# Kernel tuning notes

Measured on AMD Instinct MI355X. Metric: run time of the kernel, lower is better.

The kernel has to match this reference:

```python
import jax, jax.numpy as jnp
import numpy as np

N = 50000      # n_nodes
E = 800000     # edges (before self-loops)
IN = 128       # in_dim
HID = 32       # hidden_dim (per-head out channels)
HEADS = 4
EMB = 128      # embed_dim
LAYERS = 3
NEG_SLOPE = 0.2  # PyG GATv2 default leaky_relu slope


def _layer_norm(x, g, b):
    mu = jnp.mean(x, axis=-1, keepdims=True)
    var = jnp.var(x, axis=-1, keepdims=True)
    return g * (x - mu) / jnp.sqrt(var + 1e-5) + b


def _gatv2(h, src, dst, n, Wl, bl, Wr, br, att, bias):
    # GATv2Conv (PyG semantics, share_weights=False, concat=True).
    H, C = att.shape
    xl = (h @ Wl + bl).reshape(n, H, C)   # target (i) transform
    xr = (h @ Wr + br).reshape(n, H, C)   # source (j) transform
    x_i = xl[dst]                          # [Etot, H, C] gather
    x_j = xr[src]
    e = jax.nn.leaky_relu(x_i + x_j, NEG_SLOPE)
    logit = jnp.einsum('ehc,hc->eh', e, att)          # [Etot, H]
    # segment softmax over destination node (every node has a self-loop)
    m = jax.ops.segment_max(logit, dst, num_segments=n)
    ex = jnp.exp(logit - m[dst])
    den = jax.ops.segment_sum(ex, dst, num_segments=n)
    alpha = ex / (den[dst] + 1e-16)
    out = jax.ops.segment_sum(alpha[..., None] * x_j, dst, num_segments=n)
    return out.reshape(n, H * C) + bias


def setup_inputs() -> dict:
    key = jax.random.key(0)
    ks = iter(jax.random.split(key, 64))
    d = {}
    d['x'] = jax.random.normal(next(ks), (N, IN), jnp.float32)
    d['edge_index'] = jax.random.randint(next(ks), (2, E), 0, N, dtype=jnp.int64)

    def w(shape, fan):
        return jax.random.normal(next(ks), shape, jnp.float32) / np.float32(np.sqrt(fan))

    HC = HID * HEADS
    d['W_in'] = w((IN, HID), IN); d['b_in'] = jnp.zeros((HID,), jnp.float32)
    for i in range(LAYERS):
        ic = HID if i == 0 else HC
        d[f'Wl{i}'] = w((ic, HC), ic); d[f'bl{i}'] = jnp.zeros((HC,), jnp.float32)
        d[f'Wr{i}'] = w((ic, HC), ic); d[f'br{i}'] = jnp.zeros((HC,), jnp.float32)
        d[f'att{i}'] = w((HEADS, HID), HID)
        d[f'bo{i}'] = jnp.zeros((HC,), jnp.float32)
        d[f'g{i}'] = jnp.ones((HC,), jnp.float32)
        d[f'be{i}'] = jnp.zeros((HC,), jnp.float32)
    d['W_out'] = w((HC, EMB), HC); d['b_out'] = jnp.zeros((EMB,), jnp.float32)
    return d


def reference(x, edge_index, W_in, b_in,
              Wl0, bl0, Wr0, br0, att0, bo0, g0, be0,
              Wl1, bl1, Wr1, br1, att1, bo1, g1, be1,
              Wl2, bl2, Wr2, br2, att2, bo2, g2, be2,
              W_out, b_out):
    n = x.shape[0]
    loops = jnp.arange(n, dtype=edge_index.dtype)  # add_self_loops=True
    src = jnp.concatenate([edge_index[0], loops])
    dst = jnp.concatenate([edge_index[1], loops])

    h = jax.nn.gelu(x @ W_in + b_in, approximate=False)
    layers = [(Wl0, bl0, Wr0, br0, att0, bo0, g0, be0),
              (Wl1, bl1, Wr1, br1, att1, bo1, g1, be1),
              (Wl2, bl2, Wr2, br2, att2, bo2, g2, be2)]
    for (Wl, bl, Wr, br, att, bo, g, be) in layers:
        h_new = jax.nn.gelu(_layer_norm(_gatv2(h, src, dst, n, Wl, bl, Wr, br, att, bo), g, be), approximate=False)
        h = h + h_new if h.shape == h_new.shape else h_new  # dropout = identity (eval)
    out = h @ W_out + b_out
    norm = jnp.maximum(jnp.linalg.norm(out, axis=-1, keepdims=True), 1e-12)
    return out / norm
```

## Files before the change

### kernel.cpp

```cpp
#include <hip/hip_runtime.h>
#include <hip/hip_bf16.h>
#include <math.h>

#define N_NODES 50000
#define N_EDGES 800000
#define IN_DIM  128
#define HC_DIM  128
#define HID_C   32
#define SCAN_NB 196
#define LOG2E   1.4426950408889634f

typedef __attribute__((ext_vector_type(8))) short short8;
typedef __attribute__((ext_vector_type(4))) float f32x4;
typedef _Float16 hf8 __attribute__((ext_vector_type(8)));
typedef unsigned int uint4v __attribute__((ext_vector_type(4)));

__device__ __forceinline__ float gelu_f(float x){
    return 0.5f*x*(1.0f + erff(x*0.7071067811865475f));
}

__device__ __forceinline__ void split2(float f, short& h, short& l){
    __hip_bfloat16 bh = __float2bfloat16(f);
    float r = f - __bfloat162float(bh);
    __hip_bfloat16 blo = __float2bfloat16(r);
    h = *reinterpret_cast<short*>(&bh);
    l = *reinterpret_cast<short*>(&blo);
}
__device__ __forceinline__ unsigned short f2h(float f){
    _Float16 h = (_Float16)f;
    return __builtin_bit_cast(unsigned short, h);
}
__device__ __forceinline__ float bf2f(unsigned short u){
    return __uint_as_float(((unsigned)u)<<16);
}

__global__ __launch_bounds__(256) void k_count(const int* __restrict__ dst, int* __restrict__ cnt,
                                               int* __restrict__ rank){
    int b = blockIdx.x*1024 + threadIdx.x;
    #pragma unroll
    for(int i=0;i<4;i++){
        int e = b + i*256;
        if(e < N_EDGES) rank[e] = atomicAdd(&cnt[dst[e]], 1);
    }
}

__global__ __launch_bounds__(256) void k_scan1(const int* __restrict__ cnt, int* __restrict__ rowptr,
                                               int* __restrict__ part){
    __shared__ int sh[256];
    int t=threadIdx.x; int i=blockIdx.x*256+t;
    int v = (i<N_NODES)? cnt[i] : 0;
    sh[t]=v; __syncthreads();
    for(int off=1; off<256; off<<=1){
        int y = (t>=off)? sh[t-off] : 0;
        __syncthreads();
        sh[t] += y;
        __syncthreads();
    }
    if(i<N_NODES) rowptr[i] = sh[t]-v;
    if(t==255) part[blockIdx.x] = sh[255];
}

__global__ __launch_bounds__(256) void k_scan2(int* __restrict__ part){
    __shared__ int sh[256];
    int t=threadIdx.x;
    int v = (t<SCAN_NB)? part[t] : 0;
    sh[t]=v; __syncthreads();
    for(int off=1; off<256; off<<=1){
        int y=(t>=off)? sh[t-off]:0;
        __syncthreads();
        sh[t]+=y;
        __syncthreads();
    }
    if(t<SCAN_NB) part[t] = sh[t]-v;
}

__global__ __launch_bounds__(256) void k_scan3(int* __restrict__ rowptr, const int* __restrict__ part){
    int t=threadIdx.x; int i=blockIdx.x*256+t;
    if(i<N_NODES) rowptr[i] += part[blockIdx.x];
    if(i==0) rowptr[N_NODES]=N_EDGES;
}

__global__ __launch_bounds__(256) void k_fill(const int* __restrict__ src, const int* __restrict__ dst,
                                              const int* __restrict__ rowptr, const int* __restrict__ rank,
                                              int* __restrict__ col){
    int b = blockIdx.x*1024 + threadIdx.x;
    #pragma unroll
    for(int i=0;i<4;i++){
        int e = b + i*256;
        if(e < N_EDGES) col[rowptr[dst[e]] + rank[e]] = src[e];
    }
}

__global__ __launch_bounds__(256) void k_splitW(const float* __restrict__ W0, const float* __restrict__ W1,
                                                const float* __restrict__ W2, const float* __restrict__ W3,
                                                const float* __restrict__ W4, const float* __restrict__ W5,
                                                const float* __restrict__ W6, short* __restrict__ WT){
    int bx = blockIdx.x;
    int m, kc;
    if(bx < 2){ m = bx; kc = 0; }
    else { m = 2 + (bx-2)/4; kc = (bx-2)&3; }
    const float* src; int K; size_t off;
    switch(m){
        case 0: src=W0; K=32;  off=0;      break;
        case 1: src=W1; K=32;  off=8192;   break;
        case 2: src=W2; K=128; off=16384;  break;
        case 3: src=W3; K=128; off=49152;  break;
        case 4: src=W4; K=128; off=81920;  break;
        case 5: src=W5; K=128; off=114688; break;
        default:src=W6; K=128; off=147456; break;
    }
    short* hi = WT + off;
    short* lo = hi + (size_t)K*HC_DIM;
    #pragma unroll
    for(int i=0;i<16;i++){
        int idx = threadIdx.x + i*256;
        int k = kc*32 + (idx>>7);
        int n = idx & 127;
        float f = src[(size_t)k*HC_DIM + n];
        short h,l; split2(f,h,l);
        hi[(size_t)n*K + k] = h;
        lo[(size_t)n*K + k] = l;
    }
}

__global__ __launch_bounds__(256) void k_gemm_in(const float* __restrict__ x, const float* __restrict__ W,
                                                 const float* __restrict__ b,
                                                 short* __restrict__ hhi, short* __restrict__ hlo){
    int id = blockIdx.x*256+threadIdx.x;
    int r = id>>5, c = id&31;
    const float4* x4 = (const float4*)(x + (size_t)r*IN_DIM);
    float acc=0.f;
    #pragma unroll 8
    for(int k=0;k<IN_DIM/4;k++){
        float4 xv = x4[k];
        acc = fmaf(xv.x, W[(4*k  )*HID_C+c], acc);
        acc = fmaf(xv.y, W[(4*k+1)*HID_C+c], acc);
        acc = fmaf(xv.z, W[(4*k+2)*HID_C+c], acc);
        acc = fmaf(xv.w, W[(4*k+3)*HID_C+c], acc);
    }
    float v = gelu_f(acc + b[c]);
    short hh,ll; split2(v,hh,ll);
    hhi[(size_t)r*HID_C+c] = hh;
    hlo[(size_t)r*HID_C+c] = ll;
}

template<int K, bool PAIR, bool NORM>
__global__ __launch_bounds__(256) void k_mm(const short* __restrict__ Ahi, const short* __restrict__ Alo,
                                            const short* __restrict__ WTl, const float* __restrict__ bl,
                                            const short* __restrict__ WTr, const float* __restrict__ br,
                                            float* __restrict__ XLf, unsigned short* __restrict__ XLh,
                                            unsigned short* __restrict__ XR16){
    __shared__ float ssq[NORM?256:1];
    int t = threadIdx.x;
    int lane = t & 63, wave = t >> 6;
    int quad = lane >> 4, ml = lane & 15;
    int rbase = blockIdx.x * 64;

    const short* WTl_lo = WTl + (size_t)K*HC_DIM;
    const short* WTr_lo = PAIR ? (WTr + (size_t)K*HC_DIM) : nullptr;

    f32x4 accL[4][2], accR[4][2];
    #pragma unroll
    for(int i=0;i<4;i++)
        #pragma unroll
        for(int j=0;j<2;j++){ accL[i][j]=(f32x4){0,0,0,0}; accR[i][j]=(f32x4){0,0,0,0}; }

    int rowA[4];
    #pragma unroll
    for(int i=0;i<4;i++){
        int rr = rbase + 16*i + ml;
        rowA[i] = (rr < N_NODES) ? rr : (N_NODES-1);
    }

    #pragma unroll 2
    for(int c=0; c<K/32; c++){
        int k0 = c*32 + quad*8;
        short8 ah[4], al[4];
        #pragma unroll
        for(int i=0;i<4;i++){
            ah[i] = *(const short8*)(Ahi + (size_t)rowA[i]*K + k0);
            al[i] = *(const short8*)(Alo + (size_t)rowA[i]*K + k0);
        }
        #pragma unroll
        for(int j=0;j<2;j++){
            int nrow = j*64 + wave*16 + ml;
            short8 bh  = *(const short8*)(WTl    + (size_t)nrow*K + k0);
            short8 blo = *(const short8*)(WTl_lo + (size_t)nrow*K + k0);
            #pragma unroll
            for(int i=0;i<4;i++){
                accL[i][j] = __builtin_amdgcn_mfma_f32_16x16x32_bf16(ah[i], bh,  accL[i][j], 0,0,0);
                accL[i][j] = __builtin_amdgcn_mfma_f32_16x16x32_bf16(ah[i], blo, accL[i][j], 0,0,0);
                accL[i][j] = __builtin_amdgcn_mfma_f32_16x16x32_bf16(al[i], bh,  accL[i][j], 0,0,0);
            }
            if(PAIR){
                short8 ch = *(const short8*)(WTr    + (size_t)nrow*K + k0);
                short8 cl = *(const short8*)(WTr_lo + (size_t)nrow*K + k0);
                #pragma unroll
                for(int i=0;i<4;i++){
                    accR[i][j] = __builtin_amdgcn_mfma_f32_16x16x32_bf16(ah[i], ch, accR[i][j], 0,0,0);
                    accR[i][j] = __builtin_amdgcn_mfma_f32_16x16x32_bf16(ah[i], cl, accR[i][j], 0,0,0);
                    accR[i][j] = __builtin_amdgcn_mfma_f32_16x16x32_bf16(al[i], ch, accR[i][j], 0,0,0);
                }
            }
        }
    }

    int col0 = wave*16 + ml, col1 = 64 + wave*16 + ml;
    float bL0 = bl[col0], bL1 = bl[col1];

    if(NORM){
        #pragma unroll
        for(int i=0;i<4;i++){
            #pragma unroll
            for(int rr=0;rr<4;rr++){
                float v0 = accL[i][0][rr] + bL0;
                float v1 = accL[i][1][rr] + bL1;
                float p = v0*v0 + v1*v1;
                p += __shfl_xor(p,1); p += __shfl_xor(p,2);
                p += __shfl_xor(p,4); p += __shfl_xor(p,8);
                if(ml==0) ssq[wave*64 + 16*i + quad*4 + rr] = p;
            }
        }
        __syncthreads();
        #pragma unroll
        for(int i=0;i<4;i++){
            #pragma unroll
            for(int rr=0;rr<4;rr++){
                int row = 16*i + quad*4 + rr;
                int grr = rbase + row;
                if(grr < N_NODES){
                    float tot = ssq[row] + ssq[64+row] + ssq[128+row] + ssq[192+row];
                    float inv = 1.0f / fmaxf(sqrtf(tot), 1e-12f);
                    XLf[(size_t)grr*HC_DIM + col0] = (accL[i][0][rr] + bL0) * inv;
                    XLf[(size_t)grr*HC_DIM + col1] = (accL[i][1][rr] + bL1) * inv;
                }
            }
        }
    } else {
        float bR0 = PAIR ? br[col0] : 0.f, bR1 = PAIR ? br[col1] : 0.f;
        #pragma unroll
        for(int i=0;i<4;i++){
            #pragma unroll
            for(int rr=0;rr<4;rr++){
                int grr = rbase + 16*i + quad*4 + rr;
                if(grr < N_NODES){
                    XLh[(size_t)grr*HC_DIM + col0] = f2h(accL[i][0][rr] + bL0);
                    XLh[(size_t)grr*HC_DIM + col1] = f2h(accL[i][1][rr] + bL1);
                    if(PAIR){
                        XR16[(size_t)grr*HC_DIM + col0] = f2h(accR[i][0][rr] + bR0);
                        XR16[(size_t)grr*HC_DIM + col1] = f2h(accR[i][1][rr] + bR1);
                    }
                }
            }
        }
    }
}

__global__ __launch_bounds__(256) void k_node(const unsigned short* __restrict__ XLH, const unsigned short* __restrict__ XR,
    const int* __restrict__ rowptr, const int* __restrict__ colidx,
    const float* __restrict__ att, const float* __restrict__ bo,
    const float* __restrict__ gg, const float* __restrict__ be,
    const short* __restrict__ hold_hi, const short* __restrict__ hold_lo,
    short* __restrict__ hi_out, short* __restrict__ lo_out)
{
    int wave=threadIdx.x>>6, lane=threadIdx.x&63;
    int node = blockIdx.x*4+wave;
    int qd = lane >> 4, cl = lane & 15;
    int c8 = cl << 3;
    int ch2 = c8 + (qd<<1);

    #define H2(v,k) __builtin_shufflevector(v, v, 2*(k), 2*(k)+1)
    #define LOADH(j, xv) { xv = *(const hf8*)((const _Float16*)XR + ((size_t)((unsigned)(j)<<7)) + c8); }
#if defined(__has_builtin) && __has_builtin(__builtin_amdgcn_fdot2)
    #define LOGIT(xv, q) { \
        hf8 u_ = xlh + xv; \
        hf8 a_ = __builtin_bit_cast(hf8, __builtin_bit_cast(uint4v, u_) & 0x7fff7fffu); \
        float qa_ = __builtin_amdgcn_fdot2(H2(u_,0), H2(av6,0), 0.f, false); \
        float qb_ = __builtin_amdgcn_fdot2(H2(a_,0), H2(av4,0), 0.f, false); \
        qa_ = __builtin_amdgcn_fdot2(H2(u_,1), H2(av6,1), qa_, false); \
        qb_ = __builtin_amdgcn_fdot2(H2(a_,1), H2(av4,1), qb_, false); \
        qa_ = __builtin_amdgcn_fdot2(H2(u_,2), H2(av6,2), qa_, false); \
        qb_ = __builtin_amdgcn_fdot2(H2(a_,2), H2(av4,2), qb_, false); \
        qa_ = __builtin_amdgcn_fdot2(H2(u_,3), H2(av6,3), qa_, false); \
        qb_ = __builtin_amdgcn_fdot2(H2(a_,3), H2(av4,3), qb_, false); \
        q = qa_ + qb_; \
        q += __shfl_xor(q,1); q += __shfl_xor(q,2); }
#else
    #define LOGIT(xv, q) { \
        hf8 u_ = xlh + xv; \
        hf8 a_ = __builtin_bit_cast(hf8, __builtin_bit_cast(uint4v, u_) & 0x7fff7fffu); \
        q = 0.f; \
        _Pragma("unroll") \
        for(int k_=0;k_<8;k_++) q = fmaf((float)u_[k_], (float)av6[k_], fmaf((float)a_[k_], (float)av4[k_], q)); \
        q += __shfl_xor(q,1); q += __shfl_xor(q,2); }
#endif
    #define UPDATE4 { \
        float nm = fmaxf(m, fmaxf(fmaxf(q0,q1),fmaxf(q2,q3))); \
        float sc = exp2f(m-nm); \
        float e0=exp2f(q0-nm), e1=exp2f(q1-nm), e2=exp2f(q2-nm), e3=exp2f(q3-nm); \
        ls = fmaf(ls, sc, (e0+e1)+(e2+e3)); \
        _Pragma("unroll") \
        for(int k=0;k<8;k++) \
            acc[k] = fmaf(acc[k], sc, fmaf(e0,(float)x0[k], fmaf(e1,(float)x1[k], fmaf(e2,(float)x2[k], e3*(float)x3[k])))); \
        m = nm; }

    int beg = rowptr[node], end = rowptr[node+1];
    hf8 xlh = *(const hf8*)((const _Float16*)XLH + ((size_t)((unsigned)node<<7)) + c8);
    hf8 xs; LOADH(node, xs)
    float hres0 = 0.f, hres1 = 0.f;
    if(hold_hi){
        short2 hh = *(const short2*)(hold_hi + (size_t)node*HC_DIM + ch2);
        short2 hl = *(const short2*)(hold_lo + (size_t)node*HC_DIM + ch2);
        hres0 = bf2f((unsigned short)hh.x) + bf2f((unsigned short)hl.x);
        hres1 = bf2f((unsigned short)hh.y) + bf2f((unsigned short)hl.y);
    }

    float4 aa = *(const float4*)(att + c8);
    float4 abv = *(const float4*)(att + c8 + 4);
    float af[8] = {aa.x,aa.y,aa.z,aa.w,abv.x,abv.y,abv.z,abv.w};
    hf8 av6, av4;
    const float s6 = 0.6f*LOG2E, s4 = 0.4f*LOG2E;
    #pragma unroll
    for(int k=0;k<8;k++){
        av6[k] = (_Float16)(af[k]*s6);
        av4[k] = (_Float16)(af[k]*s4);
    }

    float qs; LOGIT(xs, qs)
    float m, ls, acc[8];
    if(qd==0){
        m = qs; ls = 1.f;
        #pragma unroll
        for(int k=0;k<8;k++) acc[k] = (float)xs[k];
    } else {
        m = -1e30f; ls = 0.f;
        #pragma unroll
        for(int k=0;k<8;k++) acc[k] = 0.f;
    }

    int P = end - beg;
    int nb = P >> 4;
    int base = beg;
    int qoff = qd << 2;
    for(int b=0; b<nb; b++, base += 16){
        int b2 = base + qoff;
        int j0 = colidx[b2], j1 = colidx[b2+1], j2 = colidx[b2+2], j3 = colidx[b2+3];
        hf8 x0,x1,x2,x3;
        LOADH(j0,x0) LOADH(j1,x1) LOADH(j2,x2) LOADH(j3,x3)
        float q0,q1,q2,q3;
        LOGIT(x0,q0) LOGIT(x1,q1) LOGIT(x2,q2) LOGIT(x3,q3)
        UPDATE4
    }
    if(base < end){
        int b2 = base + qoff;
        int j0 = (b2  <end)? colidx[b2]   : node;
        int j1 = (b2+1<end)? colidx[b2+1] : node;
        int j2 = (b2+2<end)? colidx[b2+2] : node;
        int j3 = (b2+3<end)? colidx[b2+3] : node;
        hf8 x0,x1,x2,x3;
        LOADH(j0,x0) LOADH(j1,x1) LOADH(j2,x2) LOADH(j3,x3)
        float q0,q1,q2,q3;
        LOGIT(x0,q0) LOGIT(x1,q1) LOGIT(x2,q2) LOGIT(x3,q3)
        if(b2+1>=end) q1 = -INFINITY;
        if(b2+2>=end) q2 = -INFINITY;
        if(b2+3>=end) q3 = -INFINITY;
        if(b2 < end){
            UPDATE4
        }
    }
    #undef UPDATE4
    #undef LOGIT
    #undef LOADH
    #undef H2

    #pragma unroll
    for(int mk=16; mk<=32; mk<<=1){
        float mo  = __shfl_xor(m, mk);
        float lso = __shfl_xor(ls, mk);
        float ao[8];
        #pragma unroll
        for(int k=0;k<8;k++) ao[k] = __shfl_xor(acc[k], mk);
        float nm = fmaxf(m, mo);
        float s0 = exp2f(m-nm), s1 = exp2f(mo-nm);
        ls = ls*s0 + lso*s1;
        #pragma unroll
        for(int k=0;k<8;k++) acc[k] = acc[k]*s0 + ao[k]*s1;
        m = nm;
    }

    float inv = 1.0f/ls;
    float4 b0 = *(const float4*)(bo + c8);
    float4 b1 = *(const float4*)(bo + c8 + 4);
    float bof[8] = {b0.x,b0.y,b0.z,b0.w,b1.x,b1.y,b1.z,b1.w};
    float o[8];
    #pragma unroll
    for(int k=0;k<8;k++) o[k] = fmaf(acc[k], inv, bof[k]);
    float s1v = ((o[0]+o[1])+(o[2]+o[3])) + ((o[4]+o[5])+(o[6]+o[7]));
    float s2v = o[0]*o[0];
    #pragma unroll
    for(int k=1;k<8;k++) s2v = fmaf(o[k],o[k],s2v);
    #pragma unroll
    for(int mk=1;mk<16;mk<<=1){ s1v += __shfl_xor(s1v,mk); s2v += __shfl_xor(s2v,mk); }
    float mean = s1v*(1.f/128.f);
    float var  = s2v*(1.f/128.f) - mean*mean;
    float rstd = rsqrtf(var + 1e-5f);

    float oa = (qd&2) ? ((qd&1)? o[6] : o[4]) : ((qd&1)? o[2] : o[0]);
    float ob = (qd&2) ? ((qd&1)? o[7] : o[5]) : ((qd&1)? o[3] : o[1]);
    float2 g2  = *(const float2*)(gg + ch2);
    float2 be2 = *(const float2*)(be + ch2);
    float r0 = gelu_f(fmaf(g2.x*(oa-mean), rstd, be2.x)) + hres0;
    float r1 = gelu_f(fmaf(g2.y*(ob-mean), rstd, be2.y)) + hres1;
    short h0,l0,h1,l1;
    split2(r0,h0,l0); split2(r1,h1,l1);
    *(short2*)(hi_out + (size_t)node*HC_DIM + ch2) = make_short2(h0,h1);
    *(short2*)(lo_out + (size_t)node*HC_DIM + ch2) = make_short2(l0,l1);
}

extern "C" void kernel_launch(void* const* d_in, const int* in_sizes, int n_in,
                              void* d_out, int out_size, void* d_ws, size_t ws_size,
                              hipStream_t stream)
{
    const float* x   = (const float*)d_in[0];
    const int*   ei  = (const int*)  d_in[1];
    const float* Win = (const float*)d_in[2];
    const float* bin = (const float*)d_in[3];
    const float *Wl[3], *bl[3], *Wr[3], *br[3], *att[3], *bo[3], *gg[3], *be[3];
    for(int i=0;i<3;i++){
        const int base = 4 + 8*i;
        Wl[i]=(const float*)d_in[base+0]; bl[i]=(const float*)d_in[base+1];
        Wr[i]=(const float*)d_in[base+2]; br[i]=(const float*)d_in[base+3];
        att[i]=(const float*)d_in[base+4]; bo[i]=(const float*)d_in[base+5];
        gg[i]=(const float*)d_in[base+6]; be[i]=(const float*)d_in[base+7];
    }
    const float* Wout=(const float*)d_in[28];
    const float* bout=(const float*)d_in[29];
    float* out = (float*)d_out;

    char* w = (char*)d_ws;
    unsigned short* XLH = (unsigned short*)w; w += (size_t)N_NODES*HC_DIM*2;
    unsigned short* XR16 = (unsigned short*)w; w += (size_t)N_NODES*HC_DIM*2;
    short* hAhi = (short*)w; w += (size_t)N_NODES*HC_DIM*2;
    short* hAlo = (short*)w; w += (size_t)N_NODES*HC_DIM*2;
    short* hBhi = (short*)w; w += (size_t)N_NODES*HC_DIM*2;
    short* hBlo = (short*)w; w += (size_t)N_NODES*HC_DIM*2;
    short* WT   = (short*)w; w += (size_t)180224*2;
    int* rowptr = (int*)w;  w += (size_t)(N_NODES+2)*4;
    int* cursor = (int*)w;  w += (size_t)N_NODES*4;
    int* colidx = (int*)w;  w += (size_t)N_EDGES*4;
    int* rank   = (int*)w;  w += (size_t)N_EDGES*4;
    int* part   = (int*)w;  w += 256*4;

    const int* srcp = ei;
    const int* dstp = ei + N_EDGES;

    const short* WTl0 = WT + 0;      const short* WTr0 = WT + 8192;
    const short* WTl1 = WT + 16384;  const short* WTr1 = WT + 49152;
    const short* WTl2 = WT + 81920;  const short* WTr2 = WT + 114688;
    const short* WTo  = WT + 147456;

    k_splitW<<<22,256,0,stream>>>(Wl[0],Wr[0],Wl[1],Wr[1],Wl[2],Wr[2],Wout, WT);
    hipMemsetAsync(cursor, 0, (size_t)N_NODES*4, stream);
    k_count <<<782,256, 0, stream>>>(dstp, cursor, rank);
    k_scan1 <<<SCAN_NB,256,0,stream>>>(cursor, rowptr, part);
    k_scan2 <<<1,   256, 0, stream>>>(part);
    k_scan3 <<<SCAN_NB,256,0,stream>>>(rowptr, part);
    k_fill  <<<782,256, 0, stream>>>(srcp, dstp, rowptr, rank, colidx);
    k_gemm_in<<<6250,256,0,stream>>>(x, Win, bin, hAhi, hAlo);

    k_mm<32,true,false><<<782,256,0,stream>>>(hAhi, hAlo, WTl0, bl[0], WTr0, br[0],
                                              nullptr, XLH, XR16);
    k_node<<<12500,256,0,stream>>>(XLH,XR16,rowptr,colidx,att[0],bo[0],gg[0],be[0],
                                   (const short*)nullptr, (const short*)nullptr, hBhi, hBlo);

    k_mm<128,true,false><<<782,256,0,stream>>>(hBhi, hBlo, WTl1, bl[1], WTr1, br[1],
                                               nullptr, XLH, XR16);
    k_node<<<12500,256,0,stream>>>(XLH,XR16,rowptr,colidx,att[1],bo[1],gg[1],be[1],
                                   hBhi, hBlo, hAhi, hAlo);

    k_mm<128,true,false><<<782,256,0,stream>>>(hAhi, hAlo, WTl2, bl[2], WTr2, br[2],
                                               nullptr, XLH, XR16);
    k_node<<<12500,256,0,stream>>>(XLH,XR16,rowptr,colidx,att[2],bo[2],gg[2],be[2],
                                   hAhi, hAlo, hBhi, hBlo);

    k_mm<128,false,true><<<782,256,0,stream>>>(hBhi, hBlo, WTo, bout, nullptr, nullptr,
                                               out, nullptr, nullptr);
}
```

Measured before the change: 543.8 us.

## Stage GEMM tiles in LDS and make node kernel grid-stride persistent

The projection GEMM now stages A and weight tiles (hi/lo splits) through padded shared memory per 32-wide K chunk, so each block loads weights once instead of every wave reading them from global memory. The per-node attention kernel becomes a grid-stride loop over 2048 blocks, hoisting the attention-vector, bias and layernorm parameter loads out of the per-node work. In exchange the GEMM adds two barriers per chunk with no double buffering, and the node kernel has fewer resident blocks to hide gather latency.

```diff
diff --git a/kernel.cpp b/kernel.cpp
--- a/kernel.cpp
+++ b/kernel.cpp
@@ -150,7 +150,13 @@
                                             const short* __restrict__ WTr, const float* __restrict__ br,
                                             float* __restrict__ XLf, unsigned short* __restrict__ XLh,
                                             unsigned short* __restrict__ XR16){
+    constexpr int LDS_K = 40;
+    constexpr int NCH = K / 32;
+    __shared__ short As_hi[64*LDS_K], As_lo[64*LDS_K];
+    __shared__ short Bh0[128*LDS_K], Bl0[128*LDS_K];
+    __shared__ short Bh1[PAIR?128*LDS_K:1], Bl1[PAIR?128*LDS_K:1];
     __shared__ float ssq[NORM?256:1];
+
     int t = threadIdx.x;
     int lane = t & 63, wave = t >> 6;
     int quad = lane >> 4, ml = lane & 15;
@@ -165,27 +171,40 @@
         #pragma unroll
         for(int j=0;j<2;j++){ accL[i][j]=(f32x4){0,0,0,0}; accR[i][j]=(f32x4){0,0,0,0}; }
 
-    int rowA[4];
-    #pragma unroll
-    for(int i=0;i<4;i++){
-        int rr = rbase + 16*i + ml;
-        rowA[i] = (rr < N_NODES) ? rr : (N_NODES-1);
-    }
-
-    #pragma unroll 2
-    for(int c=0; c<K/32; c++){
-        int k0 = c*32 + quad*8;
+    int r = t >> 2, seg = t & 3;
+    int gr = rbase + r; if(gr >= N_NODES) gr = N_NODES-1;
+
+    for(int c=0; c<NCH; c++){
+        if(c) __syncthreads();
+        size_t ka = (size_t)gr*K + c*32 + seg*8;
+        *(short8*)(As_hi + r*LDS_K + seg*8) = *(const short8*)(Ahi + ka);
+        *(short8*)(As_lo + r*LDS_K + seg*8) = *(const short8*)(Alo + ka);
+        #pragma unroll
+        for(int u=0; u<2; u++){
+            int uu = t + u*256;
+            int n = uu >> 2, sg = uu & 3;
+            size_t kw = (size_t)n*K + c*32 + sg*8;
+            *(short8*)(Bh0 + n*LDS_K + sg*8) = *(const short8*)(WTl + kw);
+            *(short8*)(Bl0 + n*LDS_K + sg*8) = *(const short8*)(WTl_lo + kw);
+            if(PAIR){
+                *(short8*)(Bh1 + n*LDS_K + sg*8) = *(const short8*)(WTr + kw);
+                *(short8*)(Bl1 + n*LDS_K + sg*8) = *(const short8*)(WTr_lo + kw);
+            }
+        }
+        __syncthreads();
+
+        int k0 = quad*8;
         short8 ah[4], al[4];
         #pragma unroll
         for(int i=0;i<4;i++){
-            ah[i] = *(const short8*)(Ahi + (size_t)rowA[i]*K + k0);
-            al[i] = *(const short8*)(Alo + (size_t)rowA[i]*K + k0);
+            ah[i] = *(const short8*)(As_hi + (16*i + ml)*LDS_K + k0);
+            al[i] = *(const short8*)(As_lo + (16*i + ml)*LDS_K + k0);
         }
         #pragma unroll
         for(int j=0;j<2;j++){
             int nrow = j*64 + wave*16 + ml;
-            short8 bh  = *(const short8*)(WTl    + (size_t)nrow*K + k0);
-            short8 blo = *(const short8*)(WTl_lo + (size_t)nrow*K + k0);
+            short8 bh = *(const short8*)(Bh0 + nrow*LDS_K + k0);
+            short8 blo = *(const short8*)(Bl0 + nrow*LDS_K + k0);
             #pragma unroll
             for(int i=0;i<4;i++){
                 accL[i][j] = __builtin_amdgcn_mfma_f32_16x16x32_bf16(ah[i], bh,  accL[i][j], 0,0,0);
@@ -193,8 +212,8 @@
                 accL[i][j] = __builtin_amdgcn_mfma_f32_16x16x32_bf16(al[i], bh,  accL[i][j], 0,0,0);
             }
             if(PAIR){
-                short8 ch = *(const short8*)(WTr    + (size_t)nrow*K + k0);
-                short8 cl = *(const short8*)(WTr_lo + (size_t)nrow*K + k0);
+                short8 ch = *(const short8*)(Bh1 + nrow*LDS_K + k0);
+                short8 cl = *(const short8*)(Bl1 + nrow*LDS_K + k0);
                 #pragma unroll
                 for(int i=0;i<4;i++){
                     accR[i][j] = __builtin_amdgcn_mfma_f32_16x16x32_bf16(ah[i], ch, accR[i][j], 0,0,0);
@@ -264,10 +283,25 @@
     short* __restrict__ hi_out, short* __restrict__ lo_out)
 {
     int wave=threadIdx.x>>6, lane=threadIdx.x&63;
-    int node = blockIdx.x*4+wave;
     int qd = lane >> 4, cl = lane & 15;
     int c8 = cl << 3;
     int ch2 = c8 + (qd<<1);
+
+    float4 aa = *(const float4*)(att + c8);
+    float4 abv = *(const float4*)(att + c8 + 4);
+    float af[8] = {aa.x,aa.y,aa.z,aa.w,abv.x,abv.y,abv.z,abv.w};
+    hf8 av6, av4;
+    const float s6 = 0.6f*LOG2E, s4 = 0.4f*LOG2E;
+    #pragma unroll
+    for(int k=0;k<8;k++){
+        av6[k] = (_Float16)(af[k]*s6);
+        av4[k] = (_Float16)(af[k]*s4);
+    }
+    float4 b0 = *(const float4*)(bo + c8);
+    float4 b1 = *(const float4*)(bo + c8 + 4);
+    float bof[8] = {b0.x,b0.y,b0.z,b0.w,b1.x,b1.y,b1.z,b1.w};
+    float2 g2  = *(const float2*)(gg + ch2);
+    float2 be2 = *(const float2*)(be + ch2);
 
     #define H2(v,k) __builtin_shufflevector(v, v, 2*(k), 2*(k)+1)
     #define LOADH(j, xv) { xv = *(const hf8*)((const _Float16*)XR + ((size_t)((unsigned)(j)<<7)) + c8); }
@@ -304,117 +338,105 @@
             acc[k] = fmaf(acc[k], sc, fmaf(e0,(float)x0[k], fmaf(e1,(float)x1[k], fmaf(e2,(float)x2[k], e3*(float)x3[k])))); \
         m = nm; }
 
-    int beg = rowptr[node], end = rowptr[node+1];
-    hf8 xlh = *(const hf8*)((const _Float16*)XLH + ((size_t)((unsigned)node<<7)) + c8);
-    hf8 xs; LOADH(node, xs)
-    float hres0 = 0.f, hres1 = 0.f;
-    if(hold_hi){
-        short2 hh = *(const short2*)(hold_hi + (size_t)node*HC_DIM + ch2);
-        short2 hl = *(const short2*)(hold_lo + (size_t)node*HC_DIM + ch2);
-        hres0 = bf2f((unsigned short)hh.x) + bf2f((unsigned short)hl.x);
-        hres1 = bf2f((unsigned short)hh.y) + bf2f((unsigned short)hl.y);
-    }
-
-    float4 aa = *(const float4*)(att + c8);
-    float4 abv = *(const float4*)(att + c8 + 4);
-    float af[8] = {aa.x,aa.y,aa.z,aa.w,abv.x,abv.y,abv.z,abv.w};
-    hf8 av6, av4;
-    const float s6 = 0.6f*LOG2E, s4 = 0.4f*LOG2E;
-    #pragma unroll
-    for(int k=0;k<8;k++){
-        av6[k] = (_Float16)(af[k]*s6);
-        av4[k] = (_Float16)(af[k]*s4);
-    }
-
-    float qs; LOGIT(xs, qs)
-    float m, ls, acc[8];
-    if(qd==0){
-        m = qs; ls = 1.f;
-        #pragma unroll
-        for(int k=0;k<8;k++) acc[k] = (float)xs[k];
-    } else {
-        m = -1e30f; ls = 0.f;
-        #pragma unroll
-        for(int k=0;k<8;k++) acc[k] = 0.f;
-    }
-
-    int P = end - beg;
-    int nb = P >> 4;
-    int base = beg;
-    int qoff = qd << 2;
-    for(int b=0; b<nb; b++, base += 16){
-        int b2 = base + qoff;
-        int j0 = colidx[b2], j1 = colidx[b2+1], j2 = colidx[b2+2], j3 = colidx[b2+3];
-        hf8 x0,x1,x2,x3;
-        LOADH(j0,x0) LOADH(j1,x1) LOADH(j2,x2) LOADH(j3,x3)
-        float q0,q1,q2,q3;
-        LOGIT(x0,q0) LOGIT(x1,q1) LOGIT(x2,q2) LOGIT(x3,q3)
-        UPDATE4
-    }
-    if(base < end){
-        int b2 = base + qoff;
-        int j0 = (b2  <end)? colidx[b2]   : node;
-        int j1 = (b2+1<end)? colidx[b2+1] : node;
-        int j2 = (b2+2<end)? colidx[b2+2] : node;
-        int j3 = (b2+3<end)? colidx[b2+3] : node;
-        hf8 x0,x1,x2,x3;
-        LOADH(j0,x0) LOADH(j1,x1) LOADH(j2,x2) LOADH(j3,x3)
-        float q0,q1,q2,q3;
-        LOGIT(x0,q0) LOGIT(x1,q1) LOGIT(x2,q2) LOGIT(x3,q3)
-        if(b2+1>=end) q1 = -INFINITY;
-        if(b2+2>=end) q2 = -INFINITY;
-        if(b2+3>=end) q3 = -INFINITY;
-        if(b2 < end){
+    int nstep = gridDim.x << 2;
+    for(int node = (blockIdx.x<<2) + wave; node < N_NODES; node += nstep){
+
+        int beg = rowptr[node], end = rowptr[node+1];
+        hf8 xlh = *(const hf8*)((const _Float16*)XLH + ((size_t)((unsigned)node<<7)) + c8);
+        hf8 xs; LOADH(node, xs)
+        float hres0 = 0.f, hres1 = 0.f;
+        if(hold_hi){
+            short2 hh = *(const short2*)(hold_hi + (size_t)node*HC_DIM + ch2);
+            short2 hl = *(const short2*)(hold_lo + (size_t)node*HC_DIM + ch2);
+            hres0 = bf2f((unsigned short)hh.x) + bf2f((unsigned short)hl.x);
+            hres1 = bf2f((unsigned short)hh.y) + bf2f((unsigned short)hl.y);
+        }
+
+        float qs; LOGIT(xs, qs)
+        float m, ls, acc[8];
+        if(qd==0){
+            m = qs; ls = 1.f;
+            #pragma unroll
+            for(int k=0;k<8;k++) acc[k] = (float)xs[k];
+        } else {
+            m = -1e30f; ls = 0.f;
+            #pragma unroll
+            for(int k=0;k<8;k++) acc[k] = 0.f;
+        }
+
+        int P = end - beg;
+        int nb = P >> 4;
+        int base = beg;
+        int qoff = qd << 2;
+        for(int b=0; b<nb; b++, base += 16){
+            int b2 = base + qoff;
+            int j0 = colidx[b2], j1 = colidx[b2+1], j2 = colidx[b2+2], j3 = colidx[b2+3];
+            hf8 x0,x1,x2,x3;
+            LOADH(j0,x0) LOADH(j1,x1) LOADH(j2,x2) LOADH(j3,x3)
+            float q0,q1,q2,q3;
+            LOGIT(x0,q0) LOGIT(x1,q1) LOGIT(x2,q2) LOGIT(x3,q3)
             UPDATE4
         }
+        if(base < end){
+            int b2 = base + qoff;
+            int j0 = (b2  <end)? colidx[b2]   : node;
+            int j1 = (b2+1<end)? colidx[b2+1] : node;
+            int j2 = (b2+2<end)? colidx[b2+2] : node;
+            int j3 = (b2+3<end)? colidx[b2+3] : node;
+            hf8 x0,x1,x2,x3;
+            LOADH(j0,x0) LOADH(j1,x1) LOADH(j2,x2) LOADH(j3,x3)
+            float q0,q1,q2,q3;
+            LOGIT(x0,q0) LOGIT(x1,q1) LOGIT(x2,q2) LOGIT(x3,q3)
+            if(b2+1>=end) q1 = -INFINITY;
+            if(b2+2>=end) q2 = -INFINITY;
+            if(b2+3>=end) q3 = -INFINITY;
+            if(b2 < end){
+                UPDATE4
+            }
+        }
+
+        #pragma unroll
+        for(int mk=16; mk<=32; mk<<=1){
+            float mo  = __shfl_xor(m, mk);
+            float lso = __shfl_xor(ls, mk);
+            float ao[8];
+            #pragma unroll
+            for(int k=0;k<8;k++) ao[k] = __shfl_xor(acc[k], mk);
+            float nm = fmaxf(m, mo);
+            float s0 = exp2f(m-nm), s1 = exp2f(mo-nm);
+            ls = ls*s0 + lso*s1;
+            #pragma unroll
+            for(int k=0;k<8;k++) acc[k] = acc[k]*s0 + ao[k]*s1;
+            m = nm;
+        }
+
+        float inv = 1.0f/ls;
+        float o[8];
+        #pragma unroll
+        for(int k=0;k<8;k++) o[k] = fmaf(acc[k], inv, bof[k]);
+        float s1v = ((o[0]+o[1])+(o[2]+o[3])) + ((o[4]+o[5])+(o[6]+o[7]));
+        float s2v = o[0]*o[0];
+        #pragma unroll
+        for(int k=1;k<8;k++) s2v = fmaf(o[k],o[k],s2v);
+        #pragma unroll
+        for(int mk=1;mk<16;mk<<=1){ s1v += __shfl_xor(s1v,mk); s2v += __shfl_xor(s2v,mk); }
+        float mean = s1v*(1.f/128.f);
+        float var  = s2v*(1.f/128.f) - mean*mean;
+        float rstd = rsqrtf(var + 1e-5f);
+
+        float oa = (qd&2) ? ((qd&1)? o[6] : o[4]) : ((qd&1)? o[2] : o[0]);
+        float ob = (qd&2) ? ((qd&1)? o[7] : o[5]) : ((qd&1)? o[3] : o[1]);
+        float r0 = gelu_f(fmaf(g2.x*(oa-mean), rstd, be2.x)) + hres0;
+        float r1 = gelu_f(fmaf(g2.y*(ob-mean), rstd, be2.y)) + hres1;
+        short h0,l0,h1,l1;
+        split2(r0,h0,l0); split2(r1,h1,l1);
+        *(short2*)(hi_out + (size_t)node*HC_DIM + ch2) = make_short2(h0,h1);
+        *(short2*)(lo_out + (size_t)node*HC_DIM + ch2) = make_short2(l0,l1);
     }
     #undef UPDATE4
     #undef LOGIT
     #undef LOADH
     #undef H2
-
-    #pragma unroll
-    for(int mk=16; mk<=32; mk<<=1){
-        float mo  = __shfl_xor(m, mk);
-        float lso = __shfl_xor(ls, mk);
-        float ao[8];
-        #pragma unroll
-        for(int k=0;k<8;k++) ao[k] = __shfl_xor(acc[k], mk);
-        float nm = fmaxf(m, mo);
-        float s0 = exp2f(m-nm), s1 = exp2f(mo-nm);
-        ls = ls*s0 + lso*s1;
-        #pragma unroll
-        for(int k=0;k<8;k++) acc[k] = acc[k]*s0 + ao[k]*s1;
-        m = nm;
-    }
-
-    float inv = 1.0f/ls;
-    float4 b0 = *(const float4*)(bo + c8);
-    float4 b1 = *(const float4*)(bo + c8 + 4);
-    float bof[8] = {b0.x,b0.y,b0.z,b0.w,b1.x,b1.y,b1.z,b1.w};
-    float o[8];
-    #pragma unroll
-    for(int k=0;k<8;k++) o[k] = fmaf(acc[k], inv, bof[k]);
-    float s1v = ((o[0]+o[1])+(o[2]+o[3])) + ((o[4]+o[5])+(o[6]+o[7]));
-    float s2v = o[0]*o[0];
-    #pragma unroll
-    for(int k=1;k<8;k++) s2v = fmaf(o[k],o[k],s2v);
-    #pragma unroll
-    for(int mk=1;mk<16;mk<<=1){ s1v += __shfl_xor(s1v,mk); s2v += __shfl_xor(s2v,mk); }
-    float mean = s1v*(1.f/128.f);
-    float var  = s2v*(1.f/128.f) - mean*mean;
-    float rstd = rsqrtf(var + 1e-5f);
-
-    float oa = (qd&2) ? ((qd&1)? o[6] : o[4]) : ((qd&1)? o[2] : o[0]);
-    float ob = (qd&2) ? ((qd&1)? o[7] : o[5]) : ((qd&1)? o[3] : o[1]);
-    float2 g2  = *(const float2*)(gg + ch2);
-    float2 be2 = *(const float2*)(be + ch2);
-    float r0 = gelu_f(fmaf(g2.x*(oa-mean), rstd, be2.x)) + hres0;
-    float r1 = gelu_f(fmaf(g2.y*(ob-mean), rstd, be2.y)) + hres1;
-    short h0,l0,h1,l1;
-    split2(r0,h0,l0); split2(r1,h1,l1);
-    *(short2*)(hi_out + (size_t)node*HC_DIM + ch2) = make_short2(h0,h1);
-    *(short2*)(lo_out + (size_t)node*HC_DIM + ch2) = make_short2(l0,l1);
 }
 
 extern "C" void kernel_launch(void* const* d_in, const int* in_sizes, int n_in,
@@ -470,18 +492,18 @@
 
     k_mm<32,true,false><<<782,256,0,stream>>>(hAhi, hAlo, WTl0, bl[0], WTr0, br[0],
                                               nullptr, XLH, XR16);
-    k_node<<<12500,256,0,stream>>>(XLH,XR16,rowptr,colidx,att[0],bo[0],gg[0],be[0],
-                                   (const short*)nullptr, (const short*)nullptr, hBhi, hBlo);
+    k_node<<<2048,256,0,stream>>>(XLH,XR16,rowptr,colidx,att[0],bo[0],gg[0],be[0],
+                                  (const short*)nullptr, (const short*)nullptr, hBhi, hBlo);
 
     k_mm<128,true,false><<<782,256,0,stream>>>(hBhi, hBlo, WTl1, bl[1], WTr1, br[1],
                                                nullptr, XLH, XR16);
-    k_node<<<12500,256,0,stream>>>(XLH,XR16,rowptr,colidx,att[1],bo[1],gg[1],be[1],
-                                   hBhi, hBlo, hAhi, hAlo);
+    k_node<<<2048,256,0,stream>>>(XLH,XR16,rowptr,colidx,att[1],bo[1],gg[1],be[1],
+                                  hBhi, hBlo, hAhi, hAlo);
 
     k_mm<128,true,false><<<782,256,0,stream>>>(hAhi, hAlo, WTl2, bl[2], WTr2, br[2],
                                                nullptr, XLH, XR16);
-    k_node<<<12500,256,0,stream>>>(XLH,XR16,rowptr,colidx,att[2],bo[2],gg[2],be[2],
-                                   hAhi, hAlo, hBhi, hBlo);
+    k_node<<<2048,256,0,stream>>>(XLH,XR16,rowptr,colidx,att[2],bo[2],gg[2],be[2],
+                                  hAhi, hAlo, hBhi, hBlo);
 
     k_mm<128,false,true><<<782,256,0,stream>>>(hBhi, hBlo, WTo, bout, nullptr, nullptr,
                                                out, nullptr, nullptr);
```

New measurement: 505.2 us. 7.1% less time.
